# Performance work log

Hardware: AMD Instinct MI355X
Metric: run time of the kernel (lower is better)

Reference implementation:

```python
import jax, jax.numpy as jnp
import numpy as np

B, C, H = 16, 64, 128
W_SCALE = 0.05  # keep softmax logits in a sane range


def conv1x1_relu(x, w, b):
    # x: [B,C,H,W], w: [O,C] (1x1 conv kernel squeezed), b: [O]
    y = jnp.einsum('bchw,oc->bohw', x, w) + b[None, :, None, None]
    return jax.nn.relu(y)


def setup_inputs() -> dict:
    key = jax.random.key(0)
    ks = jax.random.split(key, 10)
    inp = {
        'x': jax.random.normal(ks[0], (B, C, H, H), dtype=jnp.float32),
        'att': jax.random.normal(ks[1], (B, C, H, H), dtype=jnp.float32),
    }
    for i in range(4):
        inp[f'w{i}'] = jax.random.normal(ks[2 + 2 * i], (C, C), dtype=jnp.float32) * W_SCALE
        inp[f'b{i}'] = jax.random.normal(ks[3 + 2 * i], (C,), dtype=jnp.float32) * W_SCALE
    return inp


def reference(x, att, w0, b0, w1, b1, w2, b2, w3, b3):
    bs, c, h, w = x.shape
    query = conv1x1_relu(x, w0, b0)    # [B,C,H,W]
    key_ = conv1x1_relu(att, w1, b1)   # [B,C,H,W]
    value = conv1x1_relu(x, w2, b2)    # [B,C,H,W]
    kt = jnp.swapaxes(key_, -2, -1)    # [B,C,W,H]
    attn1 = jax.nn.softmax(jnp.matmul(query, kt), axis=-1)  # [B,C,H,H]
    attn2 = jax.nn.softmax(jnp.matmul(kt, query), axis=-1)  # [B,C,W,W]
    out = jnp.matmul(jnp.matmul(attn1, value), attn2)       # [B,C,H,W]
    out = conv1x1_relu(out, w3, b3)
    return out.reshape(bs, -1, h, h)
```

## Files before the change

kernel.cpp:

```cpp
#include <hip/hip_runtime.h>
#include <stdint.h>

#define NB   16
#define NCH  64
#define HH   128
#define NPOS (HH*HH)

typedef short bf16x8 __attribute__((ext_vector_type(8)));
typedef float f32x4  __attribute__((ext_vector_type(4)));

__device__ __forceinline__ unsigned short f2bf(float f){
  unsigned int u = __float_as_uint(f);
  u += 0x7FFFu + ((u>>16)&1u);
  return (unsigned short)(u>>16);
}
__device__ __forceinline__ unsigned int pk2(float a, float b){
  return (unsigned int)f2bf(a) | ((unsigned int)f2bf(b)<<16);
}

__device__ __forceinline__ int swz(int row, int cb){
  return cb ^ (((row & 7) ^ ((row >> 3) & 7)) << 4);
}

__global__ __launch_bounds__(256, 4) void rc_conv_in(
    const float* __restrict__ x, const float* __restrict__ att,
    const float* __restrict__ w0, const float* __restrict__ b0,
    const float* __restrict__ w1, const float* __restrict__ b1,
    const float* __restrict__ w2, const float* __restrict__ b2,
    unsigned short* __restrict__ Qb, unsigned short* __restrict__ Kb,
    unsigned short* __restrict__ Vb)
{
  __shared__ char smem[33280];
  char* Xs  = smem;
  char* WsA = smem + 16384;
  char* WsB = smem + 24576;
  float* biasA = (float*)(smem + 32768);
  float* biasB = (float*)(smem + 33024);

  const int tid = threadIdx.x;
  const int m  = blockIdx.z;
  const int b  = blockIdx.y;
  const int pblock = blockIdx.x * 128;
  const float* src = m ? att : x;
  const float* wA  = m ? w1 : w0;
  const float* bA  = m ? b1 : b0;

  {
    int o = tid >> 2, c0 = (tid & 3) * 16;
    const float4* wr = (const float4*)(wA + o*64 + c0);
    float4 f0 = wr[0], f1 = wr[1], f2v = wr[2], f3 = wr[3];
    uint4 pa, pb;
    pa.x = pk2(f0.x,f0.y);  pa.y = pk2(f0.z,f0.w);
    pa.z = pk2(f1.x,f1.y);  pa.w = pk2(f1.z,f1.w);
    pb.x = pk2(f2v.x,f2v.y); pb.y = pk2(f2v.z,f2v.w);
    pb.z = pk2(f3.x,f3.y);  pb.w = pk2(f3.z,f3.w);
    *(uint4*)(WsA + o*128 + swz(o, c0*2))      = pa;
    *(uint4*)(WsA + o*128 + swz(o, c0*2 + 16)) = pb;
    if (m == 0){
      const float4* wr2 = (const float4*)(w2 + o*64 + c0);
      float4 g0 = wr2[0], g1 = wr2[1], g2 = wr2[2], g3 = wr2[3];
      uint4 qa, qb;
      qa.x = pk2(g0.x,g0.y); qa.y = pk2(g0.z,g0.w);
      qa.z = pk2(g1.x,g1.y); qa.w = pk2(g1.z,g1.w);
      qb.x = pk2(g2.x,g2.y); qb.y = pk2(g2.z,g2.w);
      qb.z = pk2(g3.x,g3.y); qb.w = pk2(g3.z,g3.w);
      *(uint4*)(WsB + o*128 + swz(o, c0*2))      = qa;
      *(uint4*)(WsB + o*128 + swz(o, c0*2 + 16)) = qb;
    }
  }
  if (tid < 64){
    biasA[tid] = bA[tid];
    if (m == 0) biasB[tid] = b2[tid];
  }

  const float* S = src + (size_t)b*NCH*NPOS + pblock;
  float4 xr[2][4];
  #pragma unroll
  for (int g=0; g<2; ++g){
    int unit = tid + 256*g;
    int q  = unit >> 5;
    int p4 = (unit & 31) << 2;
    #pragma unroll
    for (int j=0;j<4;j++)
      xr[g][j] = *(const float4*)(S + (size_t)(4*q+j)*NPOS + p4);
  }
  #pragma unroll
  for (int g=0; g<2; ++g){
    int unit = tid + 256*g;
    int q  = unit >> 5;
    int p4 = (unit & 31) << 2;
    const float* c0 = (const float*)&xr[g][0];
    const float* c1 = (const float*)&xr[g][1];
    const float* c2 = (const float*)&xr[g][2];
    const float* c3 = (const float*)&xr[g][3];
    #pragma unroll
    for (int u=0; u<4; ++u){
      uint2 pk;
      pk.x = pk2(c0[u], c1[u]);
      pk.y = pk2(c2[u], c3[u]);
      *(uint2*)(Xs + (p4+u)*128 + swz(p4+u, q*8)) = pk;
    }
  }
  __syncthreads();

  const int w = tid>>6, l = tid&63, lq = l>>4, lm = l&15;
  bf16x8 aQ[2], aV[2] = {};
  {
    int orow = 16*w + lm;
    aQ[0] = *(const bf16x8*)(WsA + orow*128 + swz(orow,      lq*16));
    aQ[1] = *(const bf16x8*)(WsA + orow*128 + swz(orow, 64 + lq*16));
    if (m == 0){
      aV[0] = *(const bf16x8*)(WsB + orow*128 + swz(orow,      lq*16));
      aV[1] = *(const bf16x8*)(WsB + orow*128 + swz(orow, 64 + lq*16));
    }
  }
  float bQv[4], bVv[4];
  #pragma unroll
  for (int r4=0;r4<4;r4++){
    int o = 16*w + 4*lq + r4;
    bQv[r4] = biasA[o];
    bVv[r4] = (m==0) ? biasB[o] : 0.f;
  }

  f32x4 accQ[8], accV[8];
  #pragma unroll
  for (int pt=0;pt<8;pt++){ accQ[pt]=(f32x4){0,0,0,0}; accV[pt]=(f32x4){0,0,0,0}; }
  #pragma unroll
  for (int pt=0; pt<8; ++pt){
    int prow = pt*16 + lm;
    bf16x8 bx0 = *(const bf16x8*)(Xs + prow*128 + swz(prow,      lq*16));
    bf16x8 bx1 = *(const bf16x8*)(Xs + prow*128 + swz(prow, 64 + lq*16));
    accQ[pt] = __builtin_amdgcn_mfma_f32_16x16x32_bf16(aQ[0], bx0, accQ[pt], 0,0,0);
    accQ[pt] = __builtin_amdgcn_mfma_f32_16x16x32_bf16(aQ[1], bx1, accQ[pt], 0,0,0);
    if (m == 0){
      accV[pt] = __builtin_amdgcn_mfma_f32_16x16x32_bf16(aV[0], bx0, accV[pt], 0,0,0);
      accV[pt] = __builtin_amdgcn_mfma_f32_16x16x32_bf16(aV[1], bx1, accV[pt], 0,0,0);
    }
  }

  unsigned short* dA = (m ? Kb : Qb) + (size_t)b*NCH*NPOS;
  unsigned short* dB = Vb + (size_t)b*NCH*NPOS;
  const int skw = 32*((4*w + lq) & 7);

  __syncthreads();
  #pragma unroll
  for (int pt=0; pt<8; ++pt){
    #pragma unroll
    for (int r4=0;r4<4;r4++){
      int o = 16*w + 4*lq + r4;
      int p = pt*16 + lm;
      *(unsigned short*)(Xs + o*256 + ((2*p + skw) & 255)) =
          f2bf(fmaxf(accQ[pt][r4] + bQv[r4], 0.f));
    }
  }
  __syncthreads();
  {
    int o = tid >> 2, jj = tid & 3;
    int sk2 = 32*((o>>2)&7);
    #pragma unroll
    for (int i=0;i<4;i++){
      int j = i*4 + jj;
      uint4 v = *(const uint4*)(Xs + o*256 + ((j*16 + sk2) & 255));
      *(uint4*)(dA + (size_t)o*NPOS + pblock + j*8) = v;
    }
  }
  if (m == 0){
    __syncthreads();
    #pragma unroll
    for (int pt=0; pt<8; ++pt){
      #pragma unroll
      for (int r4=0;r4<4;r4++){
        int o = 16*w + 4*lq + r4;
        int p = pt*16 + lm;
        *(unsigned short*)(Xs + o*256 + ((2*p + skw) & 255)) =
            f2bf(fmaxf(accV[pt][r4] + bVv[r4], 0.f));
      }
    }
    __syncthreads();
    int o = tid >> 2, jj = tid & 3;
    int sk2 = 32*((o>>2)&7);
    #pragma unroll
    for (int i=0;i<4;i++){
      int j = i*4 + jj;
      uint4 v = *(const uint4*)(Xs + o*256 + ((j*16 + sk2) & 255));
      *(uint4*)(dB + (size_t)o*NPOS + pblock + j*8) = v;
    }
  }
}

__global__ __launch_bounds__(512) void rc_attention_mfma(
    const unsigned short* __restrict__ Qb, const unsigned short* __restrict__ Kb,
    const unsigned short* __restrict__ Vb, unsigned short* __restrict__ Pb)
{
  extern __shared__ char lds[];
  char* B0 = lds;
  char* B1 = lds + 32768;
  char* B2 = lds + 65536;
  char* B3 = lds + 98304;
  const int tid = threadIdx.x;
  const int l  = tid & 63;
  const int w  = tid >> 6;
  const int lq = l >> 4;
  const int lm = l & 15;
  const size_t gbase = (size_t)blockIdx.x * NPOS;

  uint4 vreg[4];
  #pragma unroll
  for (int i=0;i<4;i++)
    vreg[i] = *(const uint4*)(Vb + gbase + (size_t)(tid + 512*i)*8);

  #pragma unroll
  for (int i=0;i<4;i++){
    int e = (tid + 512*i)*8;
    int row = e >> 7, col = e & 127;
    uint4 q = *(const uint4*)(Qb + gbase + e);
    uint4 k = *(const uint4*)(Kb + gbase + e);
    *(uint4*)(B0 + row*256 + swz(row, col*2)) = q;
    *(uint4*)(B1 + row*256 + swz(row, col*2)) = k;
    unsigned int qd[4] = {q.x,q.y,q.z,q.w};
    unsigned int kd[4] = {k.x,k.y,k.z,k.w};
    #pragma unroll
    for (int u=0;u<8;u++){
      unsigned short qe = (unsigned short)(qd[u>>1] >> (16*(u&1)));
      unsigned short ke = (unsigned short)(kd[u>>1] >> (16*(u&1)));
      int tr = col + u;
      *(unsigned short*)(B2 + tr*256 + swz(tr, row*2)) = qe;
      *(unsigned short*)(B3 + tr*256 + swz(tr, row*2)) = ke;
    }
  }
  __syncthreads();

  f32x4 acc1[8];
  #pragma unroll
  for (int t=0;t<8;t++) acc1[t] = (f32x4){0.f,0.f,0.f,0.f};
  {
    bf16x8 bq[4];
    #pragma unroll
    for (int kk=0;kk<4;kk++){
      int r = 16*w + lm;
      bq[kk] = *(const bf16x8*)(B0 + r*256 + swz(r, kk*64 + lq*16));
    }
    #pragma unroll
    for (int kk=0;kk<4;kk++){
      #pragma unroll
      for (int jt=0;jt<8;jt++){
        int jr = jt*16 + lm;
        bf16x8 ak = *(const bf16x8*)(B1 + jr*256 + swz(jr, kk*64 + lq*16));
        acc1[jt] = __builtin_amdgcn_mfma_f32_16x16x32_bf16(ak, bq[kk], acc1[jt], 0,0,0);
      }
    }
  }
  unsigned int a1p[8][2];
  {
    float mx = -1e30f;
    #pragma unroll
    for (int t=0;t<8;t++)
      mx = fmaxf(mx, fmaxf(fmaxf(acc1[t][0], acc1[t][1]), fmaxf(acc1[t][2], acc1[t][3])));
    mx = fmaxf(mx, __shfl_xor(mx, 16));
    mx = fmaxf(mx, __shfl_xor(mx, 32));
    float sum = 0.f;
    #pragma unroll
    for (int t=0;t<8;t++){
      #pragma unroll
      for (int r4=0;r4<4;r4++){ float e = __expf(acc1[t][r4] - mx); acc1[t][r4] = e; sum += e; }
    }
    sum += __shfl_xor(sum, 16);
    sum += __shfl_xor(sum, 32);
    float inv = 1.f/sum;
    #pragma unroll
    for (int t=0;t<8;t++){
      a1p[t][0] = pk2(acc1[t][0]*inv, acc1[t][1]*inv);
      a1p[t][1] = pk2(acc1[t][2]*inv, acc1[t][3]*inv);
    }
  }

  f32x4 acc2[8];
  #pragma unroll
  for (int t=0;t<8;t++) acc2[t] = (f32x4){0.f,0.f,0.f,0.f};
  {
    bf16x8 akt[4];
    #pragma unroll
    for (int kk=0;kk<4;kk++){
      int ir = 16*w + lm;
      akt[kk] = *(const bf16x8*)(B3 + ir*256 + swz(ir, kk*64 + lq*16));
    }
    #pragma unroll
    for (int kk=0;kk<4;kk++){
      #pragma unroll
      for (int ct=0;ct<8;ct++){
        int jr = ct*16 + lm;
        bf16x8 bqt = *(const bf16x8*)(B2 + jr*256 + swz(jr, kk*64 + lq*16));
        acc2[ct] = __builtin_amdgcn_mfma_f32_16x16x32_bf16(akt[kk], bqt, acc2[ct], 0,0,0);
      }
    }
  }
  unsigned int a2p[8][2];
  {
    float m0=-1e30f, m1=-1e30f, m2=-1e30f, m3=-1e30f;
    #pragma unroll
    for (int t=0;t<8;t++){
      m0 = fmaxf(m0, acc2[t][0]); m1 = fmaxf(m1, acc2[t][1]);
      m2 = fmaxf(m2, acc2[t][2]); m3 = fmaxf(m3, acc2[t][3]);
    }
    #pragma unroll
    for (int d=1; d<16; d<<=1){
      m0 = fmaxf(m0, __shfl_xor(m0,d)); m1 = fmaxf(m1, __shfl_xor(m1,d));
      m2 = fmaxf(m2, __shfl_xor(m2,d)); m3 = fmaxf(m3, __shfl_xor(m3,d));
    }
    float s0=0.f, s1=0.f, s2=0.f, s3=0.f;
    #pragma unroll
    for (int t=0;t<8;t++){
      float e0 = __expf(acc2[t][0]-m0); acc2[t][0]=e0; s0 += e0;
      float e1 = __expf(acc2[t][1]-m1); acc2[t][1]=e1; s1 += e1;
      float e2 = __expf(acc2[t][2]-m2); acc2[t][2]=e2; s2 += e2;
      float e3 = __expf(acc2[t][3]-m3); acc2[t][3]=e3; s3 += e3;
    }
    #pragma unroll
    for (int d=1; d<16; d<<=1){
      s0 += __shfl_xor(s0,d); s1 += __shfl_xor(s1,d);
      s2 += __shfl_xor(s2,d); s3 += __shfl_xor(s3,d);
    }
    float i0=1.f/s0, i1=1.f/s1, i2=1.f/s2, i3=1.f/s3;
    #pragma unroll
    for (int t=0;t<8;t++){
      a2p[t][0] = pk2(acc2[t][0]*i0, acc2[t][1]*i1);
      a2p[t][1] = pk2(acc2[t][2]*i2, acc2[t][3]*i3);
    }
  }

  __syncthreads();

  {
    int r = 16*w + lm;
    #pragma unroll
    for (int t=0;t<8;t++)
      *(uint2*)(B3 + r*256 + swz(r, t*32 + lq*8)) = make_uint2(a1p[t][0], a1p[t][1]);
  }
  #pragma unroll
  for (int t=0;t<8;t++){
    int jr = t*16 + lm;
    *(uint2*)(B2 + jr*256 + swz(jr, 32*w + lq*8)) = make_uint2(a2p[t][0], a2p[t][1]);
  }
  #pragma unroll
  for (int i=0;i<4;i++){
    int e = (tid + 512*i)*8;
    int row = e>>7, col = e&127;
    unsigned int vd[4] = {vreg[i].x, vreg[i].y, vreg[i].z, vreg[i].w};
    #pragma unroll
    for (int u=0;u<8;u++){
      unsigned short ve = (unsigned short)(vd[u>>1] >> (16*(u&1)));
      int tr = col + u;
      *(unsigned short*)(B1 + tr*256 + swz(tr, row*2)) = ve;
    }
  }
  __syncthreads();

  f32x4 acc3[8];
  #pragma unroll
  for (int t=0;t<8;t++) acc3[t] = (f32x4){0.f,0.f,0.f,0.f};
  {
    bf16x8 av[4];
    #pragma unroll
    for (int kk=0;kk<4;kk++){
      int jr = 16*w + lm;
      av[kk] = *(const bf16x8*)(B1 + jr*256 + swz(jr, kk*64 + lq*16));
    }
    #pragma unroll
    for (int kk=0;kk<4;kk++){
      #pragma unroll
      for (int rt=0;rt<8;rt++){
        int rr = rt*16 + lm;
        bf16x8 ba = *(const bf16x8*)(B3 + rr*256 + swz(rr, kk*64 + lq*16));
        acc3[rt] = __builtin_amdgcn_mfma_f32_16x16x32_bf16(av[kk], ba, acc3[rt], 0,0,0);
      }
    }
  }
  #pragma unroll
  for (int rt=0;rt<8;rt++){
    int rr = rt*16 + lm;
    unsigned int p0 = pk2(acc3[rt][0], acc3[rt][1]);
    unsigned int p1 = pk2(acc3[rt][2], acc3[rt][3]);
    *(uint2*)(B0 + rr*256 + swz(rr, 32*w + lq*8)) = make_uint2(p0, p1);
  }
  __syncthreads();

  f32x4 acc4[8];
  #pragma unroll
  for (int t=0;t<8;t++) acc4[t] = (f32x4){0.f,0.f,0.f,0.f};
  {
    bf16x8 am[4];
    #pragma unroll
    for (int kk=0;kk<4;kk++){
      int rr = 16*w + lm;
      am[kk] = *(const bf16x8*)(B0 + rr*256 + swz(rr, kk*64 + lq*16));
    }
    #pragma unroll
    for (int kk=0;kk<4;kk++){
      #pragma unroll
      for (int ct=0;ct<8;ct++){
        int jr = ct*16 + lm;
        bf16x8 ba2 = *(const bf16x8*)(B2 + jr*256 + swz(jr, kk*64 + lq*16));
        acc4[ct] = __builtin_amdgcn_mfma_f32_16x16x32_bf16(am[kk], ba2, acc4[ct], 0,0,0);
      }
    }
  }
  unsigned short* pout = Pb + gbase;
  #pragma unroll
  for (int ct=0;ct<8;ct++){
    #pragma unroll
    for (int r4=0;r4<4;r4++){
      int rr = 16*w + lq*4 + r4;
      pout[rr*HH + ct*16 + lm] = f2bf(acc4[ct][r4]);
    }
  }
}

__global__ __launch_bounds__(256, 6) void rc_conv_out(
    const unsigned short* __restrict__ Pb, const float* __restrict__ w3,
    const float* __restrict__ b3, float* __restrict__ out)
{
  __shared__ char smem[24832];
  char* Xs = smem;
  char* Ws = smem + 16384;
  float* bias = (float*)(smem + 24576);

  const int tid = threadIdx.x;
  const int b  = blockIdx.y;
  const int pblock = blockIdx.x * 128;

  {
    int o = tid >> 2, c0 = (tid & 3) * 16;
    const float4* wr = (const float4*)(w3 + o*64 + c0);
    float4 f0 = wr[0], f1 = wr[1], f2v = wr[2], f3 = wr[3];
    uint4 pa, pb;
    pa.x = pk2(f0.x,f0.y);  pa.y = pk2(f0.z,f0.w);
    pa.z = pk2(f1.x,f1.y);  pa.w = pk2(f1.z,f1.w);
    pb.x = pk2(f2v.x,f2v.y); pb.y = pk2(f2v.z,f2v.w);
    pb.z = pk2(f3.x,f3.y);  pb.w = pk2(f3.z,f3.w);
    *(uint4*)(Ws + o*128 + swz(o, c0*2))      = pa;
    *(uint4*)(Ws + o*128 + swz(o, c0*2 + 16)) = pb;
  }
  if (tid < 64) bias[tid] = b3[tid];

  const unsigned short* S = Pb + (size_t)b*NCH*NPOS + pblock;
  uint2 pr[2][4];
  #pragma unroll
  for (int g=0; g<2; ++g){
    int unit = tid + 256*g;
    int q  = unit >> 5;
    int p4 = (unit & 31) << 2;
    #pragma unroll
    for (int j=0;j<4;j++)
      pr[g][j] = *(const uint2*)(S + (size_t)(4*q+j)*NPOS + p4);
  }
  #pragma unroll
  for (int g=0; g<2; ++g){
    int unit = tid + 256*g;
    int q  = unit >> 5;
    int p4 = (unit & 31) << 2;
    const unsigned short* e0 = (const unsigned short*)&pr[g][0];
    const unsigned short* e1 = (const unsigned short*)&pr[g][1];
    const unsigned short* e2 = (const unsigned short*)&pr[g][2];
    const unsigned short* e3 = (const unsigned short*)&pr[g][3];
    #pragma unroll
    for (int u=0; u<4; ++u){
      uint2 pk;
      pk.x = (unsigned int)e0[u] | ((unsigned int)e1[u]<<16);
      pk.y = (unsigned int)e2[u] | ((unsigned int)e3[u]<<16);
      *(uint2*)(Xs + (p4+u)*128 + swz(p4+u, q*8)) = pk;
    }
  }
  __syncthreads();

  const int w = tid>>6, l = tid&63, lq = l>>4, lm = l&15;
  bf16x8 aW[2];
  {
    int orow = 16*w + lm;
    aW[0] = *(const bf16x8*)(Ws + orow*128 + swz(orow,      lq*16));
    aW[1] = *(const bf16x8*)(Ws + orow*128 + swz(orow, 64 + lq*16));
  }
  float bv[4];
  #pragma unroll
  for (int r4=0;r4<4;r4++) bv[r4] = bias[16*w + 4*lq + r4];

  float* dst = out + (size_t)b*NCH*NPOS;
  #pragma unroll
  for (int pt=0; pt<8; ++pt){
    int prow = pt*16 + lm;
    bf16x8 bx0 = *(const bf16x8*)(Xs + prow*128 + swz(prow,      lq*16));
    bf16x8 bx1 = *(const bf16x8*)(Xs + prow*128 + swz(prow, 64 + lq*16));
    f32x4 acc = (f32x4){0.f,0.f,0.f,0.f};
    acc = __builtin_amdgcn_mfma_f32_16x16x32_bf16(aW[0], bx0, acc, 0,0,0);
    acc = __builtin_amdgcn_mfma_f32_16x16x32_bf16(aW[1], bx1, acc, 0,0,0);
    int p = pblock + pt*16 + lm;
    #pragma unroll
    for (int r4=0;r4<4;r4++){
      int o = 16*w + 4*lq + r4;
      dst[(size_t)o*NPOS + p] = fmaxf(acc[r4] + bv[r4], 0.f);
    }
  }
}

extern "C" void kernel_launch(void* const* d_in, const int* in_sizes, int n_in,
                              void* d_out, int out_size, void* d_ws, size_t ws_size,
                              hipStream_t stream)
{
  const float* x   = (const float*)d_in[0];
  const float* att = (const float*)d_in[1];
  const float* w0  = (const float*)d_in[2]; const float* b0 = (const float*)d_in[3];
  const float* w1  = (const float*)d_in[4]; const float* b1 = (const float*)d_in[5];
  const float* w2  = (const float*)d_in[6]; const float* b2 = (const float*)d_in[7];
  const float* w3  = (const float*)d_in[8]; const float* b3 = (const float*)d_in[9];

  const size_t NM = (size_t)NB*NCH*NPOS;
  unsigned short* Qb = (unsigned short*)d_ws;
  unsigned short* Kb = Qb + NM;
  unsigned short* Vb = Kb + NM;
  unsigned short* Pb = Vb + NM;
  float* out = (float*)d_out;

  (void)hipFuncSetAttribute((const void*)rc_attention_mfma,
                            hipFuncAttributeMaxDynamicSharedMemorySize, 131072);

  rc_conv_in<<<dim3(128, NB, 2), 256, 0, stream>>>(x, att, w0,b0, w1,b1, w2,b2,
                                                   Qb, Kb, Vb);

  rc_attention_mfma<<<dim3(NB*NCH), 512, 131072, stream>>>(Qb, Kb, Vb, Pb);

  rc_conv_out<<<dim3(128, NB), 256, 0, stream>>>(Pb, w3, b3, out);
}
```

Measured before the change: 118.9 us.

## Process two attention planes per block with prefetch, packed transposes, direct weight loads

The attention kernel now handles two (batch, channel) planes per block. It prefetches the second plane's Q/K/V into registers while computing the first, which is meant to hide global load latency behind MFMA work. Transposed LDS writes pair elements across lanes with shuffles so each write is 32 bits instead of 16, halving the number of LDS stores. The conv kernels load weights and biases straight into MFMA registers instead of staging them through shared memory, and conv_in's occupancy hint rises. The cost is higher register pressure from the extra prefetch buffers, plus half as many attention blocks, which reduces available parallelism.

Measured after the change: 158.8 us. +33.5%, slower.

```diff
diff --git a/kernel.cpp b/kernel.cpp
--- a/kernel.cpp
+++ b/kernel.cpp
@@ -17,12 +17,40 @@
 __device__ __forceinline__ unsigned int pk2(float a, float b){
   return (unsigned int)f2bf(a) | ((unsigned int)f2bf(b)<<16);
 }
+__device__ __forceinline__ bf16x8 pk8(float4 a, float4 b){
+  union { bf16x8 v; unsigned int u[4]; } r;
+  r.u[0] = pk2(a.x, a.y); r.u[1] = pk2(a.z, a.w);
+  r.u[2] = pk2(b.x, b.y); r.u[3] = pk2(b.z, b.w);
+  return r.v;
+}
 
 __device__ __forceinline__ int swz(int row, int cb){
   return cb ^ (((row & 7) ^ ((row >> 3) & 7)) << 4);
 }
 
-__global__ __launch_bounds__(256, 4) void rc_conv_in(
+__device__ __forceinline__ uint4 shfl_xor16(uint4 v){
+  uint4 r;
+  r.x = (unsigned int)__shfl_xor((int)v.x, 16);
+  r.y = (unsigned int)__shfl_xor((int)v.y, 16);
+  r.z = (unsigned int)__shfl_xor((int)v.z, 16);
+  r.w = (unsigned int)__shfl_xor((int)v.w, 16);
+  return r;
+}
+__device__ __forceinline__ unsigned short elem16(uint4 v, int u){
+  unsigned int d = (&v.x)[u>>1];
+  return (unsigned short)((u&1) ? (d>>16) : (d&0xffffu));
+}
+
+#define TWRITE(BUF, MINE, PART, rowv, colv)                          \
+  { _Pragma("unroll")                                                \
+    for (int u=0; u<8; ++u){                                         \
+      int tr = (colv) + u;                                           \
+      unsigned int pkv = (unsigned int)elem16((MINE),u) |            \
+                         ((unsigned int)elem16((PART),u)<<16);       \
+      *(unsigned int*)((BUF) + tr*256 + swz(tr, (rowv)*2)) = pkv;    \
+    } }
+
+__global__ __launch_bounds__(256, 6) void rc_conv_in(
     const float* __restrict__ x, const float* __restrict__ att,
     const float* __restrict__ w0, const float* __restrict__ b0,
     const float* __restrict__ w1, const float* __restrict__ b1,
@@ -30,48 +58,35 @@
     unsigned short* __restrict__ Qb, unsigned short* __restrict__ Kb,
     unsigned short* __restrict__ Vb)
 {
-  __shared__ char smem[33280];
-  char* Xs  = smem;
-  char* WsA = smem + 16384;
-  char* WsB = smem + 24576;
-  float* biasA = (float*)(smem + 32768);
-  float* biasB = (float*)(smem + 33024);
+  __shared__ char Xs[16384];
 
   const int tid = threadIdx.x;
   const int m  = blockIdx.z;
   const int b  = blockIdx.y;
   const int pblock = blockIdx.x * 128;
   const float* src = m ? att : x;
-  const float* wA  = m ? w1 : w0;
-  const float* bA  = m ? b1 : b0;
-
+  const int w = tid>>6, l = tid&63, lq = l>>4, lm = l&15;
+  const int orow = 16*w + lm;
+
+  const float* wAp = (m ? w1 : w0) + orow*64;
+  bf16x8 aQ[2], aV[2] = {};
   {
-    int o = tid >> 2, c0 = (tid & 3) * 16;
-    const float4* wr = (const float4*)(wA + o*64 + c0);
-    float4 f0 = wr[0], f1 = wr[1], f2v = wr[2], f3 = wr[3];
-    uint4 pa, pb;
-    pa.x = pk2(f0.x,f0.y);  pa.y = pk2(f0.z,f0.w);
-    pa.z = pk2(f1.x,f1.y);  pa.w = pk2(f1.z,f1.w);
-    pb.x = pk2(f2v.x,f2v.y); pb.y = pk2(f2v.z,f2v.w);
-    pb.z = pk2(f3.x,f3.y);  pb.w = pk2(f3.z,f3.w);
-    *(uint4*)(WsA + o*128 + swz(o, c0*2))      = pa;
-    *(uint4*)(WsA + o*128 + swz(o, c0*2 + 16)) = pb;
+    float4 a0 = *(const float4*)(wAp + lq*8);
+    float4 a1 = *(const float4*)(wAp + lq*8 + 4);
+    float4 a2 = *(const float4*)(wAp + 32 + lq*8);
+    float4 a3 = *(const float4*)(wAp + 32 + lq*8 + 4);
+    aQ[0] = pk8(a0, a1); aQ[1] = pk8(a2, a3);
     if (m == 0){
-      const float4* wr2 = (const float4*)(w2 + o*64 + c0);
-      float4 g0 = wr2[0], g1 = wr2[1], g2 = wr2[2], g3 = wr2[3];
-      uint4 qa, qb;
-      qa.x = pk2(g0.x,g0.y); qa.y = pk2(g0.z,g0.w);
-      qa.z = pk2(g1.x,g1.y); qa.w = pk2(g1.z,g1.w);
-      qb.x = pk2(g2.x,g2.y); qb.y = pk2(g2.z,g2.w);
-      qb.z = pk2(g3.x,g3.y); qb.w = pk2(g3.z,g3.w);
-      *(uint4*)(WsB + o*128 + swz(o, c0*2))      = qa;
-      *(uint4*)(WsB + o*128 + swz(o, c0*2 + 16)) = qb;
-    }
-  }
-  if (tid < 64){
-    biasA[tid] = bA[tid];
-    if (m == 0) biasB[tid] = b2[tid];
-  }
+      const float* wBp = w2 + orow*64;
+      float4 g0 = *(const float4*)(wBp + lq*8);
+      float4 g1 = *(const float4*)(wBp + lq*8 + 4);
+      float4 g2 = *(const float4*)(wBp + 32 + lq*8);
+      float4 g3 = *(const float4*)(wBp + 32 + lq*8 + 4);
+      aV[0] = pk8(g0, g1); aV[1] = pk8(g2, g3);
+    }
+  }
+  float4 bQ4 = *(const float4*)((m ? b1 : b0) + 16*w + 4*lq);
+  float4 bV4 = (m==0) ? *(const float4*)(b2 + 16*w + 4*lq) : (float4){0,0,0,0};
 
   const float* S = src + (size_t)b*NCH*NPOS + pblock;
   float4 xr[2][4];
@@ -102,25 +117,6 @@
     }
   }
   __syncthreads();
-
-  const int w = tid>>6, l = tid&63, lq = l>>4, lm = l&15;
-  bf16x8 aQ[2], aV[2] = {};
-  {
-    int orow = 16*w + lm;
-    aQ[0] = *(const bf16x8*)(WsA + orow*128 + swz(orow,      lq*16));
-    aQ[1] = *(const bf16x8*)(WsA + orow*128 + swz(orow, 64 + lq*16));
-    if (m == 0){
-      aV[0] = *(const bf16x8*)(WsB + orow*128 + swz(orow,      lq*16));
-      aV[1] = *(const bf16x8*)(WsB + orow*128 + swz(orow, 64 + lq*16));
-    }
-  }
-  float bQv[4], bVv[4];
-  #pragma unroll
-  for (int r4=0;r4<4;r4++){
-    int o = 16*w + 4*lq + r4;
-    bQv[r4] = biasA[o];
-    bVv[r4] = (m==0) ? biasB[o] : 0.f;
-  }
 
   f32x4 accQ[8], accV[8];
   #pragma unroll
@@ -140,6 +136,8 @@
 
   unsigned short* dA = (m ? Kb : Qb) + (size_t)b*NCH*NPOS;
   unsigned short* dB = Vb + (size_t)b*NCH*NPOS;
+  const float* bQv = (const float*)&bQ4;
+  const float* bVv = (const float*)&bV4;
   const int skw = 32*((4*w + lq) & 7);
 
   __syncthreads();
@@ -188,7 +186,7 @@
   }
 }
 
-__global__ __launch_bounds__(512) void rc_attention_mfma(
+__global__ __launch_bounds__(512, 2) void rc_attention_mfma(
     const unsigned short* __restrict__ Qb, const unsigned short* __restrict__ Kb,
     const unsigned short* __restrict__ Vb, unsigned short* __restrict__ Pb)
 {
@@ -202,215 +200,236 @@
   const int w  = tid >> 6;
   const int lq = l >> 4;
   const int lm = l & 15;
-  const size_t gbase = (size_t)blockIdx.x * NPOS;
-
-  uint4 vreg[4];
-  #pragma unroll
-  for (int i=0;i<4;i++)
-    vreg[i] = *(const uint4*)(Vb + gbase + (size_t)(tid + 512*i)*8);
-
+  const bool evenh = ((l >> 4) & 1) == 0;
+  const size_t gb0 = (size_t)(blockIdx.x * 2) * NPOS;
+
+  uint4 qr[4], kr[4], vr[4], qrn[4], krn[4], vrn[4];
   #pragma unroll
   for (int i=0;i<4;i++){
-    int e = (tid + 512*i)*8;
-    int row = e >> 7, col = e & 127;
-    uint4 q = *(const uint4*)(Qb + gbase + e);
-    uint4 k = *(const uint4*)(Kb + gbase + e);
-    *(uint4*)(B0 + row*256 + swz(row, col*2)) = q;
-    *(uint4*)(B1 + row*256 + swz(row, col*2)) = k;
-    unsigned int qd[4] = {q.x,q.y,q.z,q.w};
-    unsigned int kd[4] = {k.x,k.y,k.z,k.w};
-    #pragma unroll
-    for (int u=0;u<8;u++){
-      unsigned short qe = (unsigned short)(qd[u>>1] >> (16*(u&1)));
-      unsigned short ke = (unsigned short)(kd[u>>1] >> (16*(u&1)));
-      int tr = col + u;
-      *(unsigned short*)(B2 + tr*256 + swz(tr, row*2)) = qe;
-      *(unsigned short*)(B3 + tr*256 + swz(tr, row*2)) = ke;
-    }
-  }
-  __syncthreads();
-
-  f32x4 acc1[8];
-  #pragma unroll
-  for (int t=0;t<8;t++) acc1[t] = (f32x4){0.f,0.f,0.f,0.f};
-  {
-    bf16x8 bq[4];
-    #pragma unroll
-    for (int kk=0;kk<4;kk++){
+    size_t e = (size_t)(tid + 512*i)*8;
+    qr[i] = *(const uint4*)(Qb + gb0 + e);
+    kr[i] = *(const uint4*)(Kb + gb0 + e);
+    vr[i] = *(const uint4*)(Vb + gb0 + e);
+  }
+
+  #pragma unroll
+  for (int p=0; p<2; ++p){
+    const size_t gb = gb0 + (size_t)p*NPOS;
+
+    #pragma unroll
+    for (int i=0;i<4;i++){
+      int e = (tid + 512*i)*8;
+      int row = e >> 7, col = e & 127;
+      uint4 q = qr[i], k = kr[i];
+      *(uint4*)(B0 + row*256 + swz(row, col*2)) = q;
+      *(uint4*)(B1 + row*256 + swz(row, col*2)) = k;
+      uint4 qp = shfl_xor16(q), kp = shfl_xor16(k);
+      if (evenh){
+        TWRITE(B2, q, qp, row, col);
+        TWRITE(B3, k, kp, row, col);
+      }
+    }
+    if (p == 0){
+      #pragma unroll
+      for (int i=0;i<4;i++){
+        size_t e = (size_t)(tid + 512*i)*8;
+        qrn[i] = *(const uint4*)(Qb + gb0 + NPOS + e);
+        krn[i] = *(const uint4*)(Kb + gb0 + NPOS + e);
+      }
+    }
+    __syncthreads();
+
+    f32x4 acc1[8];
+    #pragma unroll
+    for (int t=0;t<8;t++) acc1[t] = (f32x4){0.f,0.f,0.f,0.f};
+    {
+      bf16x8 bq[4];
+      #pragma unroll
+      for (int kk=0;kk<4;kk++){
+        int r = 16*w + lm;
+        bq[kk] = *(const bf16x8*)(B0 + r*256 + swz(r, kk*64 + lq*16));
+      }
+      #pragma unroll
+      for (int kk=0;kk<4;kk++){
+        #pragma unroll
+        for (int jt=0;jt<8;jt++){
+          int jr = jt*16 + lm;
+          bf16x8 ak = *(const bf16x8*)(B1 + jr*256 + swz(jr, kk*64 + lq*16));
+          acc1[jt] = __builtin_amdgcn_mfma_f32_16x16x32_bf16(ak, bq[kk], acc1[jt], 0,0,0);
+        }
+      }
+    }
+    unsigned int a1p[8][2];
+    {
+      float mx = -1e30f;
+      #pragma unroll
+      for (int t=0;t<8;t++)
+        mx = fmaxf(mx, fmaxf(fmaxf(acc1[t][0], acc1[t][1]), fmaxf(acc1[t][2], acc1[t][3])));
+      mx = fmaxf(mx, __shfl_xor(mx, 16));
+      mx = fmaxf(mx, __shfl_xor(mx, 32));
+      float sum = 0.f;
+      #pragma unroll
+      for (int t=0;t<8;t++){
+        #pragma unroll
+        for (int r4=0;r4<4;r4++){ float e = __expf(acc1[t][r4] - mx); acc1[t][r4] = e; sum += e; }
+      }
+      sum += __shfl_xor(sum, 16);
+      sum += __shfl_xor(sum, 32);
+      float inv = 1.f/sum;
+      #pragma unroll
+      for (int t=0;t<8;t++){
+        a1p[t][0] = pk2(acc1[t][0]*inv, acc1[t][1]*inv);
+        a1p[t][1] = pk2(acc1[t][2]*inv, acc1[t][3]*inv);
+      }
+    }
+
+    f32x4 acc2[8];
+    #pragma unroll
+    for (int t=0;t<8;t++) acc2[t] = (f32x4){0.f,0.f,0.f,0.f};
+    {
+      bf16x8 akt[4];
+      #pragma unroll
+      for (int kk=0;kk<4;kk++){
+        int ir = 16*w + lm;
+        akt[kk] = *(const bf16x8*)(B3 + ir*256 + swz(ir, kk*64 + lq*16));
+      }
+      #pragma unroll
+      for (int kk=0;kk<4;kk++){
+        #pragma unroll
+        for (int ct=0;ct<8;ct++){
+          int jr = ct*16 + lm;
+          bf16x8 bqt = *(const bf16x8*)(B2 + jr*256 + swz(jr, kk*64 + lq*16));
+          acc2[ct] = __builtin_amdgcn_mfma_f32_16x16x32_bf16(akt[kk], bqt, acc2[ct], 0,0,0);
+        }
+      }
+    }
+    unsigned int a2p[8][2];
+    {
+      float m0=-1e30f, m1=-1e30f, m2=-1e30f, m3=-1e30f;
+      #pragma unroll
+      for (int t=0;t<8;t++){
+        m0 = fmaxf(m0, acc2[t][0]); m1 = fmaxf(m1, acc2[t][1]);
+        m2 = fmaxf(m2, acc2[t][2]); m3 = fmaxf(m3, acc2[t][3]);
+      }
+      #pragma unroll
+      for (int d=1; d<16; d<<=1){
+        m0 = fmaxf(m0, __shfl_xor(m0,d)); m1 = fmaxf(m1, __shfl_xor(m1,d));
+        m2 = fmaxf(m2, __shfl_xor(m2,d)); m3 = fmaxf(m3, __shfl_xor(m3,d));
+      }
+      float s0=0.f, s1=0.f, s2=0.f, s3=0.f;
+      #pragma unroll
+      for (int t=0;t<8;t++){
+        float e0 = __expf(acc2[t][0]-m0); acc2[t][0]=e0; s0 += e0;
+        float e1 = __expf(acc2[t][1]-m1); acc2[t][1]=e1; s1 += e1;
+        float e2 = __expf(acc2[t][2]-m2); acc2[t][2]=e2; s2 += e2;
+        float e3 = __expf(acc2[t][3]-m3); acc2[t][3]=e3; s3 += e3;
+      }
+      #pragma unroll
+      for (int d=1; d<16; d<<=1){
+        s0 += __shfl_xor(s0,d); s1 += __shfl_xor(s1,d);
+        s2 += __shfl_xor(s2,d); s3 += __shfl_xor(s3,d);
+      }
+      float i0=1.f/s0, i1=1.f/s1, i2=1.f/s2, i3=1.f/s3;
+      #pragma unroll
+      for (int t=0;t<8;t++){
+        a2p[t][0] = pk2(acc2[t][0]*i0, acc2[t][1]*i1);
+        a2p[t][1] = pk2(acc2[t][2]*i2, acc2[t][3]*i3);
+      }
+    }
+
+    __syncthreads();
+
+    {
       int r = 16*w + lm;
-      bq[kk] = *(const bf16x8*)(B0 + r*256 + swz(r, kk*64 + lq*16));
-    }
-    #pragma unroll
-    for (int kk=0;kk<4;kk++){
-      #pragma unroll
-      for (int jt=0;jt<8;jt++){
-        int jr = jt*16 + lm;
-        bf16x8 ak = *(const bf16x8*)(B1 + jr*256 + swz(jr, kk*64 + lq*16));
-        acc1[jt] = __builtin_amdgcn_mfma_f32_16x16x32_bf16(ak, bq[kk], acc1[jt], 0,0,0);
-      }
-    }
-  }
-  unsigned int a1p[8][2];
-  {
-    float mx = -1e30f;
-    #pragma unroll
-    for (int t=0;t<8;t++)
-      mx = fmaxf(mx, fmaxf(fmaxf(acc1[t][0], acc1[t][1]), fmaxf(acc1[t][2], acc1[t][3])));
-    mx = fmaxf(mx, __shfl_xor(mx, 16));
-    mx = fmaxf(mx, __shfl_xor(mx, 32));
-    float sum = 0.f;
+      #pragma unroll
+      for (int t=0;t<8;t++)
+        *(uint2*)(B3 + r*256 + swz(r, t*32 + lq*8)) = make_uint2(a1p[t][0], a1p[t][1]);
+    }
     #pragma unroll
     for (int t=0;t<8;t++){
-      #pragma unroll
-      for (int r4=0;r4<4;r4++){ float e = __expf(acc1[t][r4] - mx); acc1[t][r4] = e; sum += e; }
-    }
-    sum += __shfl_xor(sum, 16);
-    sum += __shfl_xor(sum, 32);
-    float inv = 1.f/sum;
-    #pragma unroll
-    for (int t=0;t<8;t++){
-      a1p[t][0] = pk2(acc1[t][0]*inv, acc1[t][1]*inv);
-      a1p[t][1] = pk2(acc1[t][2]*inv, acc1[t][3]*inv);
-    }
-  }
-
-  f32x4 acc2[8];
-  #pragma unroll
-  for (int t=0;t<8;t++) acc2[t] = (f32x4){0.f,0.f,0.f,0.f};
-  {
-    bf16x8 akt[4];
-    #pragma unroll
-    for (int kk=0;kk<4;kk++){
-      int ir = 16*w + lm;
-      akt[kk] = *(const bf16x8*)(B3 + ir*256 + swz(ir, kk*64 + lq*16));
-    }
-    #pragma unroll
-    for (int kk=0;kk<4;kk++){
-      #pragma unroll
-      for (int ct=0;ct<8;ct++){
-        int jr = ct*16 + lm;
-        bf16x8 bqt = *(const bf16x8*)(B2 + jr*256 + swz(jr, kk*64 + lq*16));
-        acc2[ct] = __builtin_amdgcn_mfma_f32_16x16x32_bf16(akt[kk], bqt, acc2[ct], 0,0,0);
-      }
-    }
-  }
-  unsigned int a2p[8][2];
-  {
-    float m0=-1e30f, m1=-1e30f, m2=-1e30f, m3=-1e30f;
-    #pragma unroll
-    for (int t=0;t<8;t++){
-      m0 = fmaxf(m0, acc2[t][0]); m1 = fmaxf(m1, acc2[t][1]);
-      m2 = fmaxf(m2, acc2[t][2]); m3 = fmaxf(m3, acc2[t][3]);
-    }
-    #pragma unroll
-    for (int d=1; d<16; d<<=1){
-      m0 = fmaxf(m0, __shfl_xor(m0,d)); m1 = fmaxf(m1, __shfl_xor(m1,d));
-      m2 = fmaxf(m2, __shfl_xor(m2,d)); m3 = fmaxf(m3, __shfl_xor(m3,d));
-    }
-    float s0=0.f, s1=0.f, s2=0.f, s3=0.f;
-    #pragma unroll
-    for (int t=0;t<8;t++){
-      float e0 = __expf(acc2[t][0]-m0); acc2[t][0]=e0; s0 += e0;
-      float e1 = __expf(acc2[t][1]-m1); acc2[t][1]=e1; s1 += e1;
-      float e2 = __expf(acc2[t][2]-m2); acc2[t][2]=e2; s2 += e2;
-      float e3 = __expf(acc2[t][3]-m3); acc2[t][3]=e3; s3 += e3;
-    }
-    #pragma unroll
-    for (int d=1; d<16; d<<=1){
-      s0 += __shfl_xor(s0,d); s1 += __shfl_xor(s1,d);
-      s2 += __shfl_xor(s2,d); s3 += __shfl_xor(s3,d);
-    }
-    float i0=1.f/s0, i1=1.f/s1, i2=1.f/s2, i3=1.f/s3;
-    #pragma unroll
-    for (int t=0;t<8;t++){
-      a2p[t][0] = pk2(acc2[t][0]*i0, acc2[t][1]*i1);
-      a2p[t][1] = pk2(acc2[t][2]*i2, acc2[t][3]*i3);
-    }
-  }
-
-  __syncthreads();
-
-  {
-    int r = 16*w + lm;
-    #pragma unroll
-    for (int t=0;t<8;t++)
-      *(uint2*)(B3 + r*256 + swz(r, t*32 + lq*8)) = make_uint2(a1p[t][0], a1p[t][1]);
-  }
-  #pragma unroll
-  for (int t=0;t<8;t++){
-    int jr = t*16 + lm;
-    *(uint2*)(B2 + jr*256 + swz(jr, 32*w + lq*8)) = make_uint2(a2p[t][0], a2p[t][1]);
-  }
-  #pragma unroll
-  for (int i=0;i<4;i++){
-    int e = (tid + 512*i)*8;
-    int row = e>>7, col = e&127;
-    unsigned int vd[4] = {vreg[i].x, vreg[i].y, vreg[i].z, vreg[i].w};
-    #pragma unroll
-    for (int u=0;u<8;u++){
-      unsigned short ve = (unsigned short)(vd[u>>1] >> (16*(u&1)));
-      int tr = col + u;
-      *(unsigned short*)(B1 + tr*256 + swz(tr, row*2)) = ve;
-    }
-  }
-  __syncthreads();
-
-  f32x4 acc3[8];
-  #pragma unroll
-  for (int t=0;t<8;t++) acc3[t] = (f32x4){0.f,0.f,0.f,0.f};
-  {
-    bf16x8 av[4];
-    #pragma unroll
-    for (int kk=0;kk<4;kk++){
-      int jr = 16*w + lm;
-      av[kk] = *(const bf16x8*)(B1 + jr*256 + swz(jr, kk*64 + lq*16));
-    }
-    #pragma unroll
-    for (int kk=0;kk<4;kk++){
-      #pragma unroll
-      for (int rt=0;rt<8;rt++){
-        int rr = rt*16 + lm;
-        bf16x8 ba = *(const bf16x8*)(B3 + rr*256 + swz(rr, kk*64 + lq*16));
-        acc3[rt] = __builtin_amdgcn_mfma_f32_16x16x32_bf16(av[kk], ba, acc3[rt], 0,0,0);
-      }
-    }
-  }
-  #pragma unroll
-  for (int rt=0;rt<8;rt++){
-    int rr = rt*16 + lm;
-    unsigned int p0 = pk2(acc3[rt][0], acc3[rt][1]);
-    unsigned int p1 = pk2(acc3[rt][2], acc3[rt][3]);
-    *(uint2*)(B0 + rr*256 + swz(rr, 32*w + lq*8)) = make_uint2(p0, p1);
-  }
-  __syncthreads();
-
-  f32x4 acc4[8];
-  #pragma unroll
-  for (int t=0;t<8;t++) acc4[t] = (f32x4){0.f,0.f,0.f,0.f};
-  {
-    bf16x8 am[4];
-    #pragma unroll
-    for (int kk=0;kk<4;kk++){
-      int rr = 16*w + lm;
-      am[kk] = *(const bf16x8*)(B0 + rr*256 + swz(rr, kk*64 + lq*16));
-    }
-    #pragma unroll
-    for (int kk=0;kk<4;kk++){
-      #pragma unroll
-      for (int ct=0;ct<8;ct++){
-        int jr = ct*16 + lm;
-        bf16x8 ba2 = *(const bf16x8*)(B2 + jr*256 + swz(jr, kk*64 + lq*16));
-        acc4[ct] = __builtin_amdgcn_mfma_f32_16x16x32_bf16(am[kk], ba2, acc4[ct], 0,0,0);
-      }
-    }
-  }
-  unsigned short* pout = Pb + gbase;
-  #pragma unroll
-  for (int ct=0;ct<8;ct++){
-    #pragma unroll
-    for (int r4=0;r4<4;r4++){
-      int rr = 16*w + lq*4 + r4;
-      pout[rr*HH + ct*16 + lm] = f2bf(acc4[ct][r4]);
+      int jr = t*16 + lm;
+      *(uint2*)(B2 + jr*256 + swz(jr, 32*w + lq*8)) = make_uint2(a2p[t][0], a2p[t][1]);
+    }
+    #pragma unroll
+    for (int i=0;i<4;i++){
+      int e = (tid + 512*i)*8;
+      int row = e>>7, col = e&127;
+      uint4 v = vr[i];
+      uint4 vp = shfl_xor16(v);
+      if (evenh) TWRITE(B1, v, vp, row, col);
+    }
+    if (p == 0){
+      #pragma unroll
+      for (int i=0;i<4;i++){
+        size_t e = (size_t)(tid + 512*i)*8;
+        vrn[i] = *(const uint4*)(Vb + gb0 + NPOS + e);
+      }
+    }
+    __syncthreads();
+
+    f32x4 acc3[8];
+    #pragma unroll
+    for (int t=0;t<8;t++) acc3[t] = (f32x4){0.f,0.f,0.f,0.f};
+    {
+      bf16x8 av[4];
+      #pragma unroll
+      for (int kk=0;kk<4;kk++){
+        int jr = 16*w + lm;
+        av[kk] = *(const bf16x8*)(B1 + jr*256 + swz(jr, kk*64 + lq*16));
+      }
+      #pragma unroll
+      for (int kk=0;kk<4;kk++){
+        #pragma unroll
+        for (int rt=0;rt<8;rt++){
+          int rr = rt*16 + lm;
+          bf16x8 ba = *(const bf16x8*)(B3 + rr*256 + swz(rr, kk*64 + lq*16));
+          acc3[rt] = __builtin_amdgcn_mfma_f32_16x16x32_bf16(av[kk], ba, acc3[rt], 0,0,0);
+        }
+      }
+    }
+    #pragma unroll
+    for (int rt=0;rt<8;rt++){
+      int rr = rt*16 + lm;
+      unsigned int p0 = pk2(acc3[rt][0], acc3[rt][1]);
+      unsigned int p1 = pk2(acc3[rt][2], acc3[rt][3]);
+      *(uint2*)(B0 + rr*256 + swz(rr, 32*w + lq*8)) = make_uint2(p0, p1);
+    }
+    __syncthreads();
+
+    f32x4 acc4[8];
+    #pragma unroll
+    for (int t=0;t<8;t++) acc4[t] = (f32x4){0.f,0.f,0.f,0.f};
+    {
+      bf16x8 am[4];
+      #pragma unroll
+      for (int kk=0;kk<4;kk++){
+        int rr = 16*w + lm;
+        am[kk] = *(const bf16x8*)(B0 + rr*256 + swz(rr, kk*64 + lq*16));
+      }
+      #pragma unroll
+      for (int kk=0;kk<4;kk++){
+        #pragma unroll
+        for (int ct=0;ct<8;ct++){
+          int jr = ct*16 + lm;
+          bf16x8 ba2 = *(const bf16x8*)(B2 + jr*256 + swz(jr, kk*64 + lq*16));
+          acc4[ct] = __builtin_amdgcn_mfma_f32_16x16x32_bf16(am[kk], ba2, acc4[ct], 0,0,0);
+        }
+      }
+    }
+    unsigned short* pout = Pb + gb;
+    #pragma unroll
+    for (int ct=0;ct<8;ct++){
+      #pragma unroll
+      for (int r4=0;r4<4;r4++){
+        int rr = 16*w + lq*4 + r4;
+        pout[rr*HH + ct*16 + lm] = f2bf(acc4[ct][r4]);
+      }
+    }
+
+    if (p == 0){
+      __syncthreads();
+      #pragma unroll
+      for (int i=0;i<4;i++){ qr[i]=qrn[i]; kr[i]=krn[i]; vr[i]=vrn[i]; }
     }
   }
 }
@@ -419,28 +438,25 @@
     const unsigned short* __restrict__ Pb, const float* __restrict__ w3,
     const float* __restrict__ b3, float* __restrict__ out)
 {
-  __shared__ char smem[24832];
-  char* Xs = smem;
-  char* Ws = smem + 16384;
-  float* bias = (float*)(smem + 24576);
+  __shared__ char Xs[16384];
 
   const int tid = threadIdx.x;
   const int b  = blockIdx.y;
   const int pblock = blockIdx.x * 128;
-
+  const int w = tid>>6, l = tid&63, lq = l>>4, lm = l&15;
+  const int orow = 16*w + lm;
+
+  bf16x8 aW[2];
   {
-    int o = tid >> 2, c0 = (tid & 3) * 16;
-    const float4* wr = (const float4*)(w3 + o*64 + c0);
-    float4 f0 = wr[0], f1 = wr[1], f2v = wr[2], f3 = wr[3];
-    uint4 pa, pb;
-    pa.x = pk2(f0.x,f0.y);  pa.y = pk2(f0.z,f0.w);
-    pa.z = pk2(f1.x,f1.y);  pa.w = pk2(f1.z,f1.w);
-    pb.x = pk2(f2v.x,f2v.y); pb.y = pk2(f2v.z,f2v.w);
-    pb.z = pk2(f3.x,f3.y);  pb.w = pk2(f3.z,f3.w);
-    *(uint4*)(Ws + o*128 + swz(o, c0*2))      = pa;
-    *(uint4*)(Ws + o*128 + swz(o, c0*2 + 16)) = pb;
-  }
-  if (tid < 64) bias[tid] = b3[tid];
+    const float* wp = w3 + orow*64;
+    float4 a0 = *(const float4*)(wp + lq*8);
+    float4 a1 = *(const float4*)(wp + lq*8 + 4);
+    float4 a2 = *(const float4*)(wp + 32 + lq*8);
+    float4 a3 = *(const float4*)(wp + 32 + lq*8 + 4);
+    aW[0] = pk8(a0, a1); aW[1] = pk8(a2, a3);
+  }
+  float4 bv4 = *(const float4*)(b3 + 16*w + 4*lq);
+  const float* bv = (const float*)&bv4;
 
   const unsigned short* S = Pb + (size_t)b*NCH*NPOS + pblock;
   uint2 pr[2][4];
@@ -471,17 +487,6 @@
     }
   }
   __syncthreads();
-
-  const int w = tid>>6, l = tid&63, lq = l>>4, lm = l&15;
-  bf16x8 aW[2];
-  {
-    int orow = 16*w + lm;
-    aW[0] = *(const bf16x8*)(Ws + orow*128 + swz(orow,      lq*16));
-    aW[1] = *(const bf16x8*)(Ws + orow*128 + swz(orow, 64 + lq*16));
-  }
-  float bv[4];
-  #pragma unroll
-  for (int r4=0;r4<4;r4++) bv[r4] = bias[16*w + 4*lq + r4];
 
   float* dst = out + (size_t)b*NCH*NPOS;
   #pragma unroll
@@ -525,7 +530,7 @@
   rc_conv_in<<<dim3(128, NB, 2), 256, 0, stream>>>(x, att, w0,b0, w1,b1, w2,b2,
                                                    Qb, Kb, Vb);
 
-  rc_attention_mfma<<<dim3(NB*NCH), 512, 131072, stream>>>(Qb, Kb, Vb, Pb);
+  rc_attention_mfma<<<dim3(NB*NCH/2), 512, 131072, stream>>>(Qb, Kb, Vb, Pb);
 
   rc_conv_out<<<dim3(128, NB), 256, 0, stream>>>(Pb, w3, b3, out);
 }
```

## Process four position tiles per conv_in block with prefetched input loads

Applied to the files above, without the earlier changes.

The input 1x1 conv kernel now handles 512 positions per block in four 128-position tiles, launching 32 blocks per batch/mode instead of 128. Weights and biases are converted and loaded once per block and reused across tiles. The next tile's fp32 input is loaded into registers while the current tile's MFMA and store phases run. This cuts per-block setup and hides global load latency, at the cost of fewer blocks (less parallelism), more register pressure and an extra barrier per tile.

Result: slower. 179.0 us (+50.5%).

```diff
diff --git a/kernel.cpp b/kernel.cpp
--- a/kernel.cpp
+++ b/kernel.cpp
@@ -40,7 +40,7 @@
   const int tid = threadIdx.x;
   const int m  = blockIdx.z;
   const int b  = blockIdx.y;
-  const int pblock = blockIdx.x * 128;
+  const int pbase = blockIdx.x * 512;
   const float* src = m ? att : x;
   const float* wA  = m ? w1 : w0;
   const float* bA  = m ? b1 : b0;
@@ -73,98 +73,87 @@
     if (m == 0) biasB[tid] = b2[tid];
   }
 
-  const float* S = src + (size_t)b*NCH*NPOS + pblock;
-  float4 xr[2][4];
-  #pragma unroll
-  for (int g=0; g<2; ++g){
-    int unit = tid + 256*g;
-    int q  = unit >> 5;
-    int p4 = (unit & 31) << 2;
-    #pragma unroll
-    for (int j=0;j<4;j++)
-      xr[g][j] = *(const float4*)(S + (size_t)(4*q+j)*NPOS + p4);
-  }
-  #pragma unroll
-  for (int g=0; g<2; ++g){
-    int unit = tid + 256*g;
-    int q  = unit >> 5;
-    int p4 = (unit & 31) << 2;
-    const float* c0 = (const float*)&xr[g][0];
-    const float* c1 = (const float*)&xr[g][1];
-    const float* c2 = (const float*)&xr[g][2];
-    const float* c3 = (const float*)&xr[g][3];
-    #pragma unroll
-    for (int u=0; u<4; ++u){
-      uint2 pk;
-      pk.x = pk2(c0[u], c1[u]);
-      pk.y = pk2(c2[u], c3[u]);
-      *(uint2*)(Xs + (p4+u)*128 + swz(p4+u, q*8)) = pk;
-    }
-  }
-  __syncthreads();
-
+  const float* Sb = src + (size_t)b*NCH*NPOS;
   const int w = tid>>6, l = tid&63, lq = l>>4, lm = l&15;
-  bf16x8 aQ[2], aV[2] = {};
-  {
-    int orow = 16*w + lm;
-    aQ[0] = *(const bf16x8*)(WsA + orow*128 + swz(orow,      lq*16));
-    aQ[1] = *(const bf16x8*)(WsA + orow*128 + swz(orow, 64 + lq*16));
-    if (m == 0){
-      aV[0] = *(const bf16x8*)(WsB + orow*128 + swz(orow,      lq*16));
-      aV[1] = *(const bf16x8*)(WsB + orow*128 + swz(orow, 64 + lq*16));
-    }
-  }
-  float bQv[4], bVv[4];
-  #pragma unroll
-  for (int r4=0;r4<4;r4++){
-    int o = 16*w + 4*lq + r4;
-    bQv[r4] = biasA[o];
-    bVv[r4] = (m==0) ? biasB[o] : 0.f;
-  }
-
-  f32x4 accQ[8], accV[8];
-  #pragma unroll
-  for (int pt=0;pt<8;pt++){ accQ[pt]=(f32x4){0,0,0,0}; accV[pt]=(f32x4){0,0,0,0}; }
-  #pragma unroll
-  for (int pt=0; pt<8; ++pt){
-    int prow = pt*16 + lm;
-    bf16x8 bx0 = *(const bf16x8*)(Xs + prow*128 + swz(prow,      lq*16));
-    bf16x8 bx1 = *(const bf16x8*)(Xs + prow*128 + swz(prow, 64 + lq*16));
-    accQ[pt] = __builtin_amdgcn_mfma_f32_16x16x32_bf16(aQ[0], bx0, accQ[pt], 0,0,0);
-    accQ[pt] = __builtin_amdgcn_mfma_f32_16x16x32_bf16(aQ[1], bx1, accQ[pt], 0,0,0);
-    if (m == 0){
-      accV[pt] = __builtin_amdgcn_mfma_f32_16x16x32_bf16(aV[0], bx0, accV[pt], 0,0,0);
-      accV[pt] = __builtin_amdgcn_mfma_f32_16x16x32_bf16(aV[1], bx1, accV[pt], 0,0,0);
-    }
-  }
-
+  const int qu0 = (tid      ) >> 5, p40 = ((tid      ) & 31) << 2;
+  const int qu1 = (tid + 256) >> 5, p41 = ((tid + 256) & 31) << 2;
   unsigned short* dA = (m ? Kb : Qb) + (size_t)b*NCH*NPOS;
   unsigned short* dB = Vb + (size_t)b*NCH*NPOS;
   const int skw = 32*((4*w + lq) & 7);
 
-  __syncthreads();
-  #pragma unroll
-  for (int pt=0; pt<8; ++pt){
-    #pragma unroll
-    for (int r4=0;r4<4;r4++){
-      int o = 16*w + 4*lq + r4;
-      int p = pt*16 + lm;
-      *(unsigned short*)(Xs + o*256 + ((2*p + skw) & 255)) =
-          f2bf(fmaxf(accQ[pt][r4] + bQv[r4], 0.f));
-    }
-  }
-  __syncthreads();
-  {
-    int o = tid >> 2, jj = tid & 3;
-    int sk2 = 32*((o>>2)&7);
-    #pragma unroll
-    for (int i=0;i<4;i++){
-      int j = i*4 + jj;
-      uint4 v = *(const uint4*)(Xs + o*256 + ((j*16 + sk2) & 255));
-      *(uint4*)(dA + (size_t)o*NPOS + pblock + j*8) = v;
-    }
-  }
-  if (m == 0){
+  float4 xr[2][4];
+  #pragma unroll
+  for (int j=0;j<4;j++){
+    xr[0][j] = *(const float4*)(Sb + (size_t)(4*qu0+j)*NPOS + pbase + p40);
+    xr[1][j] = *(const float4*)(Sb + (size_t)(4*qu1+j)*NPOS + pbase + p41);
+  }
+
+  bool wloaded = false;
+  bf16x8 aQ[2] = {}, aV[2] = {};
+  float bQv[4], bVv[4];
+
+  for (int t=0; t<4; ++t){
+    #pragma unroll
+    for (int g=0; g<2; ++g){
+      int q  = g ? qu1 : qu0;
+      int p4 = g ? p41 : p40;
+      const float* c0 = (const float*)&xr[g][0];
+      const float* c1 = (const float*)&xr[g][1];
+      const float* c2 = (const float*)&xr[g][2];
+      const float* c3 = (const float*)&xr[g][3];
+      #pragma unroll
+      for (int u=0; u<4; ++u){
+        uint2 pk;
+        pk.x = pk2(c0[u], c1[u]);
+        pk.y = pk2(c2[u], c3[u]);
+        *(uint2*)(Xs + (p4+u)*128 + swz(p4+u, q*8)) = pk;
+      }
+    }
+    __syncthreads();
+
+    if (!wloaded){
+      wloaded = true;
+      int orow = 16*w + lm;
+      aQ[0] = *(const bf16x8*)(WsA + orow*128 + swz(orow,      lq*16));
+      aQ[1] = *(const bf16x8*)(WsA + orow*128 + swz(orow, 64 + lq*16));
+      if (m == 0){
+        aV[0] = *(const bf16x8*)(WsB + orow*128 + swz(orow,      lq*16));
+        aV[1] = *(const bf16x8*)(WsB + orow*128 + swz(orow, 64 + lq*16));
+      }
+      #pragma unroll
+      for (int r4=0;r4<4;r4++){
+        int o = 16*w + 4*lq + r4;
+        bQv[r4] = biasA[o];
+        bVv[r4] = (m==0) ? biasB[o] : 0.f;
+      }
+    }
+
+    f32x4 accQ[8], accV[8];
+    #pragma unroll
+    for (int pt=0;pt<8;pt++){ accQ[pt]=(f32x4){0,0,0,0}; accV[pt]=(f32x4){0,0,0,0}; }
+    #pragma unroll
+    for (int pt=0; pt<8; ++pt){
+      int prow = pt*16 + lm;
+      bf16x8 bx0 = *(const bf16x8*)(Xs + prow*128 + swz(prow,      lq*16));
+      bf16x8 bx1 = *(const bf16x8*)(Xs + prow*128 + swz(prow, 64 + lq*16));
+      accQ[pt] = __builtin_amdgcn_mfma_f32_16x16x32_bf16(aQ[0], bx0, accQ[pt], 0,0,0);
+      accQ[pt] = __builtin_amdgcn_mfma_f32_16x16x32_bf16(aQ[1], bx1, accQ[pt], 0,0,0);
+      if (m == 0){
+        accV[pt] = __builtin_amdgcn_mfma_f32_16x16x32_bf16(aV[0], bx0, accV[pt], 0,0,0);
+        accV[pt] = __builtin_amdgcn_mfma_f32_16x16x32_bf16(aV[1], bx1, accV[pt], 0,0,0);
+      }
+    }
+
+    if (t < 3){
+      #pragma unroll
+      for (int j=0;j<4;j++){
+        xr[0][j] = *(const float4*)(Sb + (size_t)(4*qu0+j)*NPOS + pbase + (t+1)*128 + p40);
+        xr[1][j] = *(const float4*)(Sb + (size_t)(4*qu1+j)*NPOS + pbase + (t+1)*128 + p41);
+      }
+    }
+
+    const int pblock = pbase + t*128;
+
     __syncthreads();
     #pragma unroll
     for (int pt=0; pt<8; ++pt){
@@ -173,18 +162,43 @@
         int o = 16*w + 4*lq + r4;
         int p = pt*16 + lm;
         *(unsigned short*)(Xs + o*256 + ((2*p + skw) & 255)) =
-            f2bf(fmaxf(accV[pt][r4] + bVv[r4], 0.f));
+            f2bf(fmaxf(accQ[pt][r4] + bQv[r4], 0.f));
       }
     }
     __syncthreads();
-    int o = tid >> 2, jj = tid & 3;
-    int sk2 = 32*((o>>2)&7);
-    #pragma unroll
-    for (int i=0;i<4;i++){
-      int j = i*4 + jj;
-      uint4 v = *(const uint4*)(Xs + o*256 + ((j*16 + sk2) & 255));
-      *(uint4*)(dB + (size_t)o*NPOS + pblock + j*8) = v;
-    }
+    {
+      int o = tid >> 2, jj = tid & 3;
+      int sk2 = 32*((o>>2)&7);
+      #pragma unroll
+      for (int i=0;i<4;i++){
+        int j = i*4 + jj;
+        uint4 v = *(const uint4*)(Xs + o*256 + ((j*16 + sk2) & 255));
+        *(uint4*)(dA + (size_t)o*NPOS + pblock + j*8) = v;
+      }
+    }
+    if (m == 0){
+      __syncthreads();
+      #pragma unroll
+      for (int pt=0; pt<8; ++pt){
+        #pragma unroll
+        for (int r4=0;r4<4;r4++){
+          int o = 16*w + 4*lq + r4;
+          int p = pt*16 + lm;
+          *(unsigned short*)(Xs + o*256 + ((2*p + skw) & 255)) =
+              f2bf(fmaxf(accV[pt][r4] + bVv[r4], 0.f));
+        }
+      }
+      __syncthreads();
+      int o = tid >> 2, jj = tid & 3;
+      int sk2 = 32*((o>>2)&7);
+      #pragma unroll
+      for (int i=0;i<4;i++){
+        int j = i*4 + jj;
+        uint4 v = *(const uint4*)(Xs + o*256 + ((j*16 + sk2) & 255));
+        *(uint4*)(dB + (size_t)o*NPOS + pblock + j*8) = v;
+      }
+    }
+    __syncthreads();
   }
 }
 
@@ -522,8 +536,8 @@
   (void)hipFuncSetAttribute((const void*)rc_attention_mfma,
                             hipFuncAttributeMaxDynamicSharedMemorySize, 131072);
 
-  rc_conv_in<<<dim3(128, NB, 2), 256, 0, stream>>>(x, att, w0,b0, w1,b1, w2,b2,
-                                                   Qb, Kb, Vb);
+  rc_conv_in<<<dim3(32, NB, 2), 256, 0, stream>>>(x, att, w0,b0, w1,b1, w2,b2,
+                                                  Qb, Kb, Vb);
 
   rc_attention_mfma<<<dim3(NB*NCH), 512, 131072, stream>>>(Qb, Kb, Vb, Pb);
 
```
